# Kernel tuning notes

Measured on AMD Instinct MI355X. Metric: run time of the kernel, lower is better.

## Reference

```python
import jax, jax.numpy as jnp
import numpy as np

N_NODES = 100000


def sage_layer(h, src, dst, w_self, w_neigh, b):
    """DGL SAGEConv with mean aggregator: fc_self(h) + fc_neigh(mean_in_neigh(h)) + b."""
    msg = h[src]  # [E, d] gather source features
    agg = jax.ops.segment_sum(msg, dst, num_segments=N_NODES)  # [N, d]
    deg = jax.ops.segment_sum(jnp.ones((src.shape[0],), h.dtype), dst, num_segments=N_NODES)
    mean = agg / jnp.maximum(deg, 1.0)[:, None]
    return h @ w_self + mean @ w_neigh + b


def setup_inputs() -> dict:
    key = jax.random.key(0)
    ks = jax.random.split(key, 12)
    N, E = N_NODES, 1600000
    in_f, hid, n_cls = 4, 128, 2

    def glorot(k, shape):
        lim = float(np.sqrt(6.0 / (shape[0] + shape[1])))
        return jax.random.uniform(k, shape, jnp.float32, -lim, lim)

    return {
        "feats": jax.random.normal(ks[0], (N, in_f), jnp.float32),
        "src": jax.random.randint(ks[1], (E,), 0, N),
        "dst": jax.random.randint(ks[2], (E,), 0, N),
        "w_self1": glorot(ks[3], (in_f, hid)),
        "w_neigh1": glorot(ks[4], (in_f, hid)),
        "b1": jnp.zeros((hid,), jnp.float32),
        "w_self2": glorot(ks[5], (hid, hid)),
        "w_neigh2": glorot(ks[6], (hid, hid)),
        "b2": jnp.zeros((hid,), jnp.float32),
        "w_out": glorot(ks[7], (hid, n_cls)),
        "b_out": jnp.zeros((n_cls,), jnp.float32),
    }


def reference(feats, src, dst, w_self1, w_neigh1, b1, w_self2, w_neigh2, b2, w_out, b_out):
    h = jax.nn.relu(sage_layer(feats, src, dst, w_self1, w_neigh1, b1))
    h = jax.nn.relu(sage_layer(h, src, dst, w_self2, w_neigh2, b2))
    return h @ w_out + b_out  # [N, num_classes] logits
```

## Files before the change

### kernel.cpp

```cpp
#include <hip/hip_runtime.h>
#include <hip/hip_bf16.h>

static constexpr int N = 100000;
static constexpr int HID = 128;
static constexpr int NBKT = (N + 127) / 128;
static constexpr int BCAP = 2560;
static constexpr int BEPB = 4096;

typedef short v8s __attribute__((ext_vector_type(8)));
typedef float v4f __attribute__((ext_vector_type(4)));
typedef unsigned short u16x8 __attribute__((ext_vector_type(8)));

static __device__ __forceinline__ unsigned short f2bf(float x) {
  unsigned u = __float_as_uint(x);
  return (unsigned short)((u + 0x7fffu + ((u >> 16) & 1u)) >> 16);
}
static __device__ __forceinline__ float bf2f(unsigned short u) {
  return __uint_as_float(((unsigned)u) << 16);
}

__global__ void k_wprep(const float* __restrict__ ws2, const float* __restrict__ wn2,
                        unsigned short* __restrict__ wp, unsigned* __restrict__ bcur) {
  int id = blockIdx.x * 64 + threadIdx.x;
  if (id < NBKT) bcur[id] = (unsigned)id * BCAP;
  int b = blockIdx.x;
  int mat = b >> 5;
  int ks = (b >> 3) & 3;
  int cf = b & 7;
  int l = threadIdx.x;
  const float* W = mat ? wn2 : ws2;
  int col = cf * 16 + (l & 15);
  int k0 = ks * 32 + (l >> 4) * 8;
  u16x8 h8, l8;
#pragma unroll
  for (int i = 0; i < 8; ++i) {
    float w = W[(k0 + i) * 128 + col];
    unsigned short h = f2bf(w);
    h8[i] = h;
    l8[i] = f2bf(w - bf2f(h));
  }
  int fhi = (ks * 4 + mat) * 8 + cf;
  int flo = (ks * 4 + mat + 2) * 8 + cf;
  *reinterpret_cast<u16x8*>(wp + fhi * 512 + l * 8) = h8;
  *reinterpret_cast<u16x8*>(wp + flo * 512 + l * 8) = l8;
}

__global__ __launch_bounds__(256) void k_bucket(const int* __restrict__ src,
                                                const int* __restrict__ dst,
                                                unsigned* __restrict__ bcur,
                                                unsigned* __restrict__ bucket, int E) {
  __shared__ unsigned hist[NBKT];
  __shared__ unsigned base[NBKT];
  for (int i = threadIdx.x; i < NBKT; i += 256) hist[i] = 0;
  __syncthreads();
  const int e0 = blockIdx.x * BEPB;
  const int n = min(e0 + BEPB, E) - e0;

  unsigned pk[16];
  int bk[16];
#pragma unroll
  for (int i = 0; i < 16; ++i) {
    int e = threadIdx.x + 256 * i;
    if (e < n) {
      int d = __builtin_nontemporal_load(dst + e0 + e);
      int s = __builtin_nontemporal_load(src + e0 + e);
      int b = d >> 7;
      pk[i] = ((unsigned)s << 7) | (unsigned)(d & 127);
      bk[i] = b;
      atomicAdd(&hist[b], 1u);
    } else {
      bk[i] = -1;
      pk[i] = 0;
    }
  }
  __syncthreads();
  for (int i = threadIdx.x; i < NBKT; i += 256) {
    unsigned h = hist[i];
    base[i] = h ? atomicAdd(&bcur[i], h) : 0u;
    hist[i] = 0;
  }
  __syncthreads();
#pragma unroll
  for (int i = 0; i < 16; ++i) {
    if (bk[i] >= 0) {
      unsigned pos = base[bk[i]] + atomicAdd(&hist[bk[i]], 1u);
      bucket[pos] = pk[i];
    }
  }
}

__global__ void k_bucketscan(const unsigned* __restrict__ bcur, unsigned* __restrict__ bbase) {
  __shared__ unsigned s[1024];
  int t = threadIdx.x;
  unsigned v = (t < NBKT) ? (bcur[t] - (unsigned)t * BCAP) : 0u;
  s[t] = v;
  __syncthreads();
  for (int off = 1; off < 1024; off <<= 1) {
    unsigned x = (t >= off) ? s[t - off] : 0u;
    __syncthreads();
    s[t] += x;
    __syncthreads();
  }
  if (t < NBKT) bbase[t] = s[t] - v;
}

__global__ __launch_bounds__(256) void k_csr(const unsigned* __restrict__ bcur,
                                             const unsigned* __restrict__ bbase,
                                             const unsigned* __restrict__ bucket,
                                             unsigned* __restrict__ cnt,
                                             unsigned* __restrict__ roff,
                                             int* __restrict__ csr) {
  const int b = blockIdx.x;
  const unsigned segbase = (unsigned)b * BCAP;
  const unsigned n = bcur[b] - segbase;
  const int v0 = b << 7;
  __shared__ unsigned h[128];
  __shared__ unsigned rowoff[128];
  __shared__ unsigned s[128];
  if (threadIdx.x < 128) h[threadIdx.x] = 0;
  __syncthreads();

  unsigned pk[10];
#pragma unroll
  for (int i = 0; i < 10; ++i) {
    unsigned idx = threadIdx.x + 256u * i;
    if (idx < n) {
      pk[i] = bucket[segbase + idx];
      atomicAdd(&h[pk[i] & 127u], 1u);
    } else {
      pk[i] = 0xffffffffu;
    }
  }
  __syncthreads();

  unsigned val = (threadIdx.x < 128) ? h[threadIdx.x] : 0u;
  if (threadIdx.x < 128) s[threadIdx.x] = val;
  __syncthreads();
  for (int off = 1; off < 128; off <<= 1) {
    unsigned x = (threadIdx.x < 128 && threadIdx.x >= off) ? s[threadIdx.x - off] : 0u;
    __syncthreads();
    if (threadIdx.x < 128) s[threadIdx.x] += x;
    __syncthreads();
  }
  if (threadIdx.x < 128) {
    int v = v0 + threadIdx.x;
    if (v < N) {
      unsigned rstart = bbase[b] + s[threadIdx.x] - val;
      rowoff[threadIdx.x] = rstart;
      roff[v] = rstart;
      cnt[v] = val;
    }
    h[threadIdx.x] = 0;
  }
  __syncthreads();

#pragma unroll
  for (int i = 0; i < 10; ++i) {
    if (pk[i] != 0xffffffffu) {
      unsigned dl = pk[i] & 127u;
      unsigned pos = rowoff[dl] + atomicAdd(&h[dl], 1u);
      csr[pos] = (int)(pk[i] >> 7);
    }
  }
}

__global__ void k_layer1(const float* __restrict__ feats, const unsigned* __restrict__ cnt,
                         const unsigned* __restrict__ roff, const int* __restrict__ csr,
                         const float* __restrict__ ws1, const float* __restrict__ wn1,
                         const float* __restrict__ b1, unsigned short* __restrict__ h1) {
  const int v = blockIdx.x * 16 + (threadIdx.x >> 4);
  const int l = threadIdx.x & 15;
  if (v >= N) return;
  const unsigned c = cnt[v];
  const unsigned start = roff[v];
  float4 acc = make_float4(0.f, 0.f, 0.f, 0.f);
  for (unsigned e = l; e < c; e += 16) {
    int s = csr[start + e];
    float4 f = *reinterpret_cast<const float4*>(feats + 4 * s);
    acc.x += f.x; acc.y += f.y; acc.z += f.z; acc.w += f.w;
  }
#pragma unroll
  for (int off = 1; off < 16; off <<= 1) {
    acc.x += __shfl_xor(acc.x, off);
    acc.y += __shfl_xor(acc.y, off);
    acc.z += __shfl_xor(acc.z, off);
    acc.w += __shfl_xor(acc.w, off);
  }
  float inv = 1.0f / fmaxf((float)c, 1.0f);
  float m0 = acc.x * inv, m1 = acc.y * inv, m2 = acc.z * inv, m3 = acc.w * inv;
  float4 fv = *reinterpret_cast<const float4*>(feats + 4 * v);
  const int c0 = l * 8;
  unsigned o[4];
#pragma unroll
  for (int half = 0; half < 2; ++half) {
    float4 bv = *reinterpret_cast<const float4*>(b1 + c0 + 4 * half);
    float ob[4] = {bv.x, bv.y, bv.z, bv.w};
#pragma unroll
    for (int k = 0; k < 4; ++k) {
      float4 wsv = *reinterpret_cast<const float4*>(ws1 + k * 128 + c0 + 4 * half);
      float4 wnv = *reinterpret_cast<const float4*>(wn1 + k * 128 + c0 + 4 * half);
      float fk = (k == 0) ? fv.x : (k == 1) ? fv.y : (k == 2) ? fv.z : fv.w;
      float mk = (k == 0) ? m0 : (k == 1) ? m1 : (k == 2) ? m2 : m3;
      ob[0] += fk * wsv.x + mk * wnv.x;
      ob[1] += fk * wsv.y + mk * wnv.y;
      ob[2] += fk * wsv.z + mk * wnv.z;
      ob[3] += fk * wsv.w + mk * wnv.w;
    }
#pragma unroll
    for (int jj = 0; jj < 2; ++jj) {
      float lo = fmaxf(ob[2 * jj], 0.f), hi = fmaxf(ob[2 * jj + 1], 0.f);
      o[2 * half + jj] = (unsigned)f2bf(lo) | (((unsigned)f2bf(hi)) << 16);
    }
  }
  *reinterpret_cast<uint4*>(h1 + (size_t)v * HID + c0) =
      make_uint4(o[0], o[1], o[2], o[3]);
}

__global__ void k_agg(const unsigned* __restrict__ cnt, const unsigned* __restrict__ roff,
                      const int* __restrict__ csr, const unsigned short* __restrict__ h1,
                      unsigned short* __restrict__ mean) {
  const int wv = threadIdx.x >> 6;
  const int lane = threadIdx.x & 63;
  const int hl = lane & 31;
  const int v = blockIdx.x * 8 + wv * 2 + (lane >> 5);
  if (v >= N) return;
  const unsigned c = cnt[v];
  const unsigned start = roff[v];
  const unsigned short* __restrict__ hrow = h1 + hl * 4;

  float a0 = 0.f, a1 = 0.f, a2 = 0.f, a3 = 0.f;
  float b0 = 0.f, b1 = 0.f, b2 = 0.f, b3 = 0.f;

  const unsigned cm = c & ~3u;
  unsigned e = 0;
  for (; e < cm; e += 4) {
    int s[4];
#pragma unroll
    for (int q = 0; q < 4; ++q) s[q] = csr[start + e + q];
    uint2 pk[4];
#pragma unroll
    for (int q = 0; q < 4; ++q)
      pk[q] = *reinterpret_cast<const uint2*>(hrow + (size_t)s[q] * HID);
#pragma unroll
    for (int q = 0; q < 4; ++q) {
      float f0 = __uint_as_float(pk[q].x << 16);
      float f1 = __uint_as_float(pk[q].x & 0xffff0000u);
      float f2 = __uint_as_float(pk[q].y << 16);
      float f3 = __uint_as_float(pk[q].y & 0xffff0000u);
      if (q & 1) { b0 += f0; b1 += f1; b2 += f2; b3 += f3; }
      else       { a0 += f0; a1 += f1; a2 += f2; a3 += f3; }
    }
  }
  for (; e < c; ++e) {
    int s = csr[start + e];
    uint2 pk = *reinterpret_cast<const uint2*>(hrow + (size_t)s * HID);
    a0 += __uint_as_float(pk.x << 16);
    a1 += __uint_as_float(pk.x & 0xffff0000u);
    a2 += __uint_as_float(pk.y << 16);
    a3 += __uint_as_float(pk.y & 0xffff0000u);
  }
  float inv = 1.0f / fmaxf((float)c, 1.0f);
  a0 = (a0 + b0) * inv; a1 = (a1 + b1) * inv;
  a2 = (a2 + b2) * inv; a3 = (a3 + b3) * inv;
  uint2 o;
  o.x = (unsigned)f2bf(a0) | (((unsigned)f2bf(a1)) << 16);
  o.y = (unsigned)f2bf(a2) | (((unsigned)f2bf(a3)) << 16);
  *reinterpret_cast<uint2*>(mean + (size_t)v * HID + hl * 4) = o;
}

__global__ __launch_bounds__(256) void k_l2_mfma(
    const unsigned short* __restrict__ h1, const unsigned short* __restrict__ mean,
    const unsigned short* __restrict__ wp, const float* __restrict__ b2,
    const float* __restrict__ wout, const float* __restrict__ bout,
    float* __restrict__ out) {
  const int l = threadIdx.x & 63;
  const int wv = threadIdx.x >> 6;
  const size_t vbase = (size_t)blockIdx.x * 256 + (size_t)wv * 64;
  const int rlane = l & 15;
  const int kg = l >> 4;

  v4f acc[4][8];
#pragma unroll
  for (int rf = 0; rf < 4; ++rf)
#pragma unroll
    for (int cf = 0; cf < 8; ++cf) acc[rf][cf] = (v4f)(0.f);

#pragma unroll
  for (int ks = 0; ks < 4; ++ks) {
    v8s ah[4], am[4];
#pragma unroll
    for (int rf = 0; rf < 4; ++rf) {
      size_t row = vbase + rf * 16 + rlane;
      if (row >= N) row = N - 1;
      size_t off = row * HID + ks * 32 + kg * 8;
      ah[rf] = *reinterpret_cast<const v8s*>(h1 + off);
      am[rf] = *reinterpret_cast<const v8s*>(mean + off);
    }
#pragma unroll
    for (int m = 0; m < 4; ++m) {
#pragma unroll
      for (int cf = 0; cf < 8; ++cf) {
        v8s bf = *reinterpret_cast<const v8s*>(wp + ((ks * 4 + m) * 8 + cf) * 512 + l * 8);
#pragma unroll
        for (int rf = 0; rf < 4; ++rf) {
          acc[rf][cf] = __builtin_amdgcn_mfma_f32_16x16x32_bf16(
              (m & 1) ? am[rf] : ah[rf], bf, acc[rf][cf], 0, 0, 0);
        }
      }
    }
  }

  float b2c[8], w0c[8], w1c[8];
#pragma unroll
  for (int cf = 0; cf < 8; ++cf) {
    int col = cf * 16 + rlane;
    b2c[cf] = b2[col];
    w0c[cf] = wout[col * 2 + 0];
    w1c[cf] = wout[col * 2 + 1];
  }
  const float bo0 = bout[0], bo1 = bout[1];
#pragma unroll
  for (int rf = 0; rf < 4; ++rf) {
#pragma unroll
    for (int j = 0; j < 4; ++j) {
      float s0 = 0.f, s1 = 0.f;
#pragma unroll
      for (int cf = 0; cf < 8; ++cf) {
        float h2 = fmaxf(acc[rf][cf][j] + b2c[cf], 0.f);
        s0 += h2 * w0c[cf];
        s1 += h2 * w1c[cf];
      }
#pragma unroll
      for (int off = 1; off < 16; off <<= 1) {
        s0 += __shfl_xor(s0, off);
        s1 += __shfl_xor(s1, off);
      }
      size_t row = vbase + rf * 16 + kg * 4 + j;
      if (row < N) {
        if (rlane == 0) out[row * 2 + 0] = s0 + bo0;
        if (rlane == 1) out[row * 2 + 1] = s1 + bo1;
      }
    }
  }
}

extern "C" void kernel_launch(void* const* d_in, const int* in_sizes, int n_in,
                              void* d_out, int out_size, void* d_ws, size_t ws_size,
                              hipStream_t stream) {
  const float* feats = (const float*)d_in[0];
  const int* src = (const int*)d_in[1];
  const int* dst = (const int*)d_in[2];
  const float* ws1 = (const float*)d_in[3];
  const float* wn1 = (const float*)d_in[4];
  const float* b1 = (const float*)d_in[5];
  const float* ws2 = (const float*)d_in[6];
  const float* wn2 = (const float*)d_in[7];
  const float* b2 = (const float*)d_in[8];
  const float* wout = (const float*)d_in[9];
  const float* bout = (const float*)d_in[10];
  float* out = (float*)d_out;
  const int E = in_sizes[1];

  char* p = (char*)d_ws;
  unsigned* bcur = (unsigned*)p;             p += 784 * 4;
  unsigned* bbase = (unsigned*)p;            p += 784 * 4;
  unsigned* bucket = (unsigned*)p;           p += (size_t)NBKT * BCAP * 4;
  int* csr = (int*)p;                        p += (size_t)E * 4;
  unsigned* cnt = (unsigned*)p;              p += (size_t)N * 4;
  unsigned* roff = (unsigned*)p;             p += (size_t)N * 4;
  unsigned short* h1 = (unsigned short*)p;   p += (size_t)N * HID * 2;
  unsigned short* mean = (unsigned short*)p; p += (size_t)N * HID * 2;
  unsigned short* wp = (unsigned short*)p;

  int bgrid = (E + BEPB - 1) / BEPB;
  k_wprep<<<64, 64, 0, stream>>>(ws2, wn2, wp, bcur);
  k_bucket<<<bgrid, 256, 0, stream>>>(src, dst, bcur, bucket, E);
  k_bucketscan<<<1, 1024, 0, stream>>>(bcur, bbase);
  k_csr<<<NBKT, 256, 0, stream>>>(bcur, bbase, bucket, cnt, roff, csr);
  k_layer1<<<(N + 15) / 16, 256, 0, stream>>>(feats, cnt, roff, csr, ws1, wn1, b1, h1);
  k_agg<<<(N + 7) / 8, 256, 0, stream>>>(cnt, roff, csr, h1, mean);
  k_l2_mfma<<<(N + 255) / 256, 256, 0, stream>>>(h1, mean, wp, b2, wout, bout, out);
}
```

Before: 181.6 us.

## Fuse neighbor mean aggregation into layer-2 MFMA kernel via LDS staging

Merges the aggregation kernel and the layer-2 MFMA/output kernel. Each 256-thread block now aggregates 64 nodes into a shared-memory tile of bf16 means, then each wave runs MFMAs on its 16 rows. This removes the global write and re-read of the N x 128 mean buffer and one launch. In exchange each wave now covers 16 rows instead of 64, so weight fragments are reloaded four times more often per row and MFMA reuse drops, and the aggregation and matmul phases are serialized inside each block.

```diff
diff --git a/kernel.cpp b/kernel.cpp
--- a/kernel.cpp
+++ b/kernel.cpp
@@ -216,96 +216,86 @@
       make_uint4(o[0], o[1], o[2], o[3]);
 }
 
-__global__ void k_agg(const unsigned* __restrict__ cnt, const unsigned* __restrict__ roff,
-                      const int* __restrict__ csr, const unsigned short* __restrict__ h1,
-                      unsigned short* __restrict__ mean) {
-  const int wv = threadIdx.x >> 6;
-  const int lane = threadIdx.x & 63;
-  const int hl = lane & 31;
-  const int v = blockIdx.x * 8 + wv * 2 + (lane >> 5);
-  if (v >= N) return;
-  const unsigned c = cnt[v];
-  const unsigned start = roff[v];
-  const unsigned short* __restrict__ hrow = h1 + hl * 4;
-
-  float a0 = 0.f, a1 = 0.f, a2 = 0.f, a3 = 0.f;
-  float b0 = 0.f, b1 = 0.f, b2 = 0.f, b3 = 0.f;
-
-  const unsigned cm = c & ~3u;
-  unsigned e = 0;
-  for (; e < cm; e += 4) {
-    int s[4];
-#pragma unroll
-    for (int q = 0; q < 4; ++q) s[q] = csr[start + e + q];
-    uint2 pk[4];
-#pragma unroll
-    for (int q = 0; q < 4; ++q)
-      pk[q] = *reinterpret_cast<const uint2*>(hrow + (size_t)s[q] * HID);
-#pragma unroll
-    for (int q = 0; q < 4; ++q) {
-      float f0 = __uint_as_float(pk[q].x << 16);
-      float f1 = __uint_as_float(pk[q].x & 0xffff0000u);
-      float f2 = __uint_as_float(pk[q].y << 16);
-      float f3 = __uint_as_float(pk[q].y & 0xffff0000u);
-      if (q & 1) { b0 += f0; b1 += f1; b2 += f2; b3 += f3; }
-      else       { a0 += f0; a1 += f1; a2 += f2; a3 += f3; }
-    }
-  }
-  for (; e < c; ++e) {
-    int s = csr[start + e];
-    uint2 pk = *reinterpret_cast<const uint2*>(hrow + (size_t)s * HID);
-    a0 += __uint_as_float(pk.x << 16);
-    a1 += __uint_as_float(pk.x & 0xffff0000u);
-    a2 += __uint_as_float(pk.y << 16);
-    a3 += __uint_as_float(pk.y & 0xffff0000u);
-  }
-  float inv = 1.0f / fmaxf((float)c, 1.0f);
-  a0 = (a0 + b0) * inv; a1 = (a1 + b1) * inv;
-  a2 = (a2 + b2) * inv; a3 = (a3 + b3) * inv;
-  uint2 o;
-  o.x = (unsigned)f2bf(a0) | (((unsigned)f2bf(a1)) << 16);
-  o.y = (unsigned)f2bf(a2) | (((unsigned)f2bf(a3)) << 16);
-  *reinterpret_cast<uint2*>(mean + (size_t)v * HID + hl * 4) = o;
-}
-
-__global__ __launch_bounds__(256) void k_l2_mfma(
-    const unsigned short* __restrict__ h1, const unsigned short* __restrict__ mean,
+__global__ __launch_bounds__(256) void k_agg_l2(
+    const unsigned* __restrict__ cnt, const unsigned* __restrict__ roff,
+    const int* __restrict__ csr, const unsigned short* __restrict__ h1,
     const unsigned short* __restrict__ wp, const float* __restrict__ b2,
     const float* __restrict__ wout, const float* __restrict__ bout,
     float* __restrict__ out) {
-  const int l = threadIdx.x & 63;
-  const int wv = threadIdx.x >> 6;
-  const size_t vbase = (size_t)blockIdx.x * 256 + (size_t)wv * 64;
-  const int rlane = l & 15;
-  const int kg = l >> 4;
-
-  v4f acc[4][8];
-#pragma unroll
-  for (int rf = 0; rf < 4; ++rf)
-#pragma unroll
-    for (int cf = 0; cf < 8; ++cf) acc[rf][cf] = (v4f)(0.f);
-
+  __shared__ unsigned short mlds[64][136];
+  const int t = threadIdx.x;
+  const int wv = t >> 6;
+  const int lane = t & 63;
+  const int hl = lane & 31;
+  const int half = lane >> 5;
+  const int vbase = blockIdx.x * 64;
+
+  const unsigned short* __restrict__ hrow = h1 + hl * 4;
+#pragma unroll 1
+  for (int p = 0; p < 8; ++p) {
+    const int vl = wv * 16 + 2 * p + half;
+    const int v = vbase + vl;
+    unsigned c = 0, start = 0;
+    if (v < N) { c = cnt[v]; start = roff[v]; }
+    float x0 = 0.f, x1 = 0.f, x2 = 0.f, x3 = 0.f;
+    float y0 = 0.f, y1 = 0.f, y2 = 0.f, y3 = 0.f;
+    const unsigned cm = c & ~3u;
+    unsigned e = 0;
+    for (; e < cm; e += 4) {
+      int s[4];
+#pragma unroll
+      for (int q = 0; q < 4; ++q) s[q] = csr[start + e + q];
+      uint2 pk[4];
+#pragma unroll
+      for (int q = 0; q < 4; ++q)
+        pk[q] = *reinterpret_cast<const uint2*>(hrow + (size_t)s[q] * HID);
+#pragma unroll
+      for (int q = 0; q < 4; ++q) {
+        float f0 = __uint_as_float(pk[q].x << 16);
+        float f1 = __uint_as_float(pk[q].x & 0xffff0000u);
+        float f2 = __uint_as_float(pk[q].y << 16);
+        float f3 = __uint_as_float(pk[q].y & 0xffff0000u);
+        if (q & 1) { y0 += f0; y1 += f1; y2 += f2; y3 += f3; }
+        else       { x0 += f0; x1 += f1; x2 += f2; x3 += f3; }
+      }
+    }
+    for (; e < c; ++e) {
+      int s = csr[start + e];
+      uint2 pk = *reinterpret_cast<const uint2*>(hrow + (size_t)s * HID);
+      x0 += __uint_as_float(pk.x << 16);
+      x1 += __uint_as_float(pk.x & 0xffff0000u);
+      x2 += __uint_as_float(pk.y << 16);
+      x3 += __uint_as_float(pk.y & 0xffff0000u);
+    }
+    float inv = 1.0f / fmaxf((float)c, 1.0f);
+    x0 = (x0 + y0) * inv; x1 = (x1 + y1) * inv;
+    x2 = (x2 + y2) * inv; x3 = (x3 + y3) * inv;
+    uint2 o;
+    o.x = (unsigned)f2bf(x0) | (((unsigned)f2bf(x1)) << 16);
+    o.y = (unsigned)f2bf(x2) | (((unsigned)f2bf(x3)) << 16);
+    *reinterpret_cast<uint2*>(&mlds[vl][hl * 4]) = o;
+  }
+  __syncthreads();
+
+  const int rlane = lane & 15;
+  const int kg = lane >> 4;
+  v4f acc[8];
+#pragma unroll
+  for (int cf = 0; cf < 8; ++cf) acc[cf] = (v4f)(0.f);
+
+  size_t hr = (size_t)vbase + wv * 16 + rlane;
+  if (hr >= N) hr = N - 1;
 #pragma unroll
   for (int ks = 0; ks < 4; ++ks) {
-    v8s ah[4], am[4];
-#pragma unroll
-    for (int rf = 0; rf < 4; ++rf) {
-      size_t row = vbase + rf * 16 + rlane;
-      if (row >= N) row = N - 1;
-      size_t off = row * HID + ks * 32 + kg * 8;
-      ah[rf] = *reinterpret_cast<const v8s*>(h1 + off);
-      am[rf] = *reinterpret_cast<const v8s*>(mean + off);
-    }
+    v8s ah = *reinterpret_cast<const v8s*>(h1 + hr * HID + ks * 32 + kg * 8);
+    v8s am = *reinterpret_cast<const v8s*>(&mlds[wv * 16 + rlane][ks * 32 + kg * 8]);
 #pragma unroll
     for (int m = 0; m < 4; ++m) {
 #pragma unroll
       for (int cf = 0; cf < 8; ++cf) {
-        v8s bf = *reinterpret_cast<const v8s*>(wp + ((ks * 4 + m) * 8 + cf) * 512 + l * 8);
-#pragma unroll
-        for (int rf = 0; rf < 4; ++rf) {
-          acc[rf][cf] = __builtin_amdgcn_mfma_f32_16x16x32_bf16(
-              (m & 1) ? am[rf] : ah[rf], bf, acc[rf][cf], 0, 0, 0);
-        }
+        v8s bf = *reinterpret_cast<const v8s*>(wp + ((ks * 4 + m) * 8 + cf) * 512 + lane * 8);
+        acc[cf] = __builtin_amdgcn_mfma_f32_16x16x32_bf16(
+            (m & 1) ? am : ah, bf, acc[cf], 0, 0, 0);
       }
     }
   }
@@ -320,26 +310,23 @@
   }
   const float bo0 = bout[0], bo1 = bout[1];
 #pragma unroll
-  for (int rf = 0; rf < 4; ++rf) {
-#pragma unroll
-    for (int j = 0; j < 4; ++j) {
-      float s0 = 0.f, s1 = 0.f;
-#pragma unroll
-      for (int cf = 0; cf < 8; ++cf) {
-        float h2 = fmaxf(acc[rf][cf][j] + b2c[cf], 0.f);
-        s0 += h2 * w0c[cf];
-        s1 += h2 * w1c[cf];
-      }
-#pragma unroll
-      for (int off = 1; off < 16; off <<= 1) {
-        s0 += __shfl_xor(s0, off);
-        s1 += __shfl_xor(s1, off);
-      }
-      size_t row = vbase + rf * 16 + kg * 4 + j;
-      if (row < N) {
-        if (rlane == 0) out[row * 2 + 0] = s0 + bo0;
-        if (rlane == 1) out[row * 2 + 1] = s1 + bo1;
-      }
+  for (int j = 0; j < 4; ++j) {
+    float s0 = 0.f, s1 = 0.f;
+#pragma unroll
+    for (int cf = 0; cf < 8; ++cf) {
+      float h2 = fmaxf(acc[cf][j] + b2c[cf], 0.f);
+      s0 += h2 * w0c[cf];
+      s1 += h2 * w1c[cf];
+    }
+#pragma unroll
+    for (int off = 1; off < 16; off <<= 1) {
+      s0 += __shfl_xor(s0, off);
+      s1 += __shfl_xor(s1, off);
+    }
+    size_t row = (size_t)vbase + wv * 16 + kg * 4 + j;
+    if (row < N) {
+      if (rlane == 0) out[row * 2 + 0] = s0 + bo0;
+      if (rlane == 1) out[row * 2 + 1] = s1 + bo1;
     }
   }
 }
@@ -369,7 +356,6 @@
   unsigned* cnt = (unsigned*)p;              p += (size_t)N * 4;
   unsigned* roff = (unsigned*)p;             p += (size_t)N * 4;
   unsigned short* h1 = (unsigned short*)p;   p += (size_t)N * HID * 2;
-  unsigned short* mean = (unsigned short*)p; p += (size_t)N * HID * 2;
   unsigned short* wp = (unsigned short*)p;
 
   int bgrid = (E + BEPB - 1) / BEPB;
@@ -378,6 +364,5 @@
   k_bucketscan<<<1, 1024, 0, stream>>>(bcur, bbase);
   k_csr<<<NBKT, 256, 0, stream>>>(bcur, bbase, bucket, cnt, roff, csr);
   k_layer1<<<(N + 15) / 16, 256, 0, stream>>>(feats, cnt, roff, csr, ws1, wn1, b1, h1);
-  k_agg<<<(N + 7) / 8, 256, 0, stream>>>(cnt, roff, csr, h1, mean);
-  k_l2_mfma<<<(N + 255) / 256, 256, 0, stream>>>(h1, mean, wp, b2, wout, bout, out);
-}
+  k_agg_l2<<<(N + 63) / 64, 256, 0, stream>>>(cnt, roff, csr, h1, wp, b2, wout, bout, out);
+}
```

Measured after the change: 191.0 us. 1.05x slower.
